# Performance work log

Measured on AMD Instinct MI355X. Metric: run time of the kernel, lower is better.

Reference implementation:

```python
import jax, jax.numpy as jnp
import numpy as np

DIM = 512
HEADS = 8
DIM_HEAD = 64
HIDDEN = HEADS * DIM_HEAD
SCALE = DIM_HEAD ** -0.5


def rmsnorm_ch(x, g):
    # F.normalize over channel dim (axis=1), then * g * sqrt(C)
    # x: [b, c, l], g: [c]
    n = jnp.maximum(jnp.linalg.norm(x, axis=1, keepdims=True), 1e-12)
    c = x.shape[1]
    return (x / n) * g[None, :, None] * (c ** 0.5)


def setup_inputs() -> dict:
    key = jax.random.key(0)
    ks = jax.random.split(key, 6)
    b, l = 8, 4096
    x = jax.random.normal(ks[0], (b, DIM, l), dtype=jnp.float32)
    g_in = jnp.ones((DIM,), dtype=jnp.float32)
    # conv1d kernel_size=1 == matmul; kaiming-ish init scale
    w_qkv = jax.random.normal(ks[1], (3 * HIDDEN, DIM), dtype=jnp.float32) * (1.0 / np.sqrt(DIM))
    w_out = jax.random.normal(ks[2], (DIM, HIDDEN), dtype=jnp.float32) * (1.0 / np.sqrt(HIDDEN))
    b_out = jax.random.normal(ks[3], (DIM,), dtype=jnp.float32) * 0.01
    g_out = jnp.ones((DIM,), dtype=jnp.float32)
    return {"x": x, "g_in": g_in, "w_qkv": w_qkv, "w_out": w_out, "b_out": b_out, "g_out": g_out}


def reference(x, g_in, w_qkv, w_out, b_out, g_out):
    b, c, l = x.shape
    residual = x
    xn = rmsnorm_ch(x, g_in)                       # [b, c, l]
    qkv = jnp.einsum('oc,bcl->bol', w_qkv, xn)     # [b, 3*hidden, l]
    q, k, v = jnp.split(qkv, 3, axis=1)            # each [b, hidden, l]
    def to_heads(t):
        return t.reshape(b, HEADS, DIM_HEAD, l)    # [b, h, d, l]
    q, k, v = to_heads(q), to_heads(k), to_heads(v)
    q = jax.nn.softmax(q, axis=2) * SCALE          # softmax over head-dim d
    k = jax.nn.softmax(k, axis=3)                  # softmax over sequence l
    context = jnp.einsum('bhdn,bhen->bhde', k, v)  # [b, h, d, e]
    out = jnp.einsum('bhde,bhdn->bhen', context, q)  # [b, h, e, l]
    out = out.reshape(b, HIDDEN, l)
    o = jnp.einsum('ch,bhl->bcl', w_out, out) + b_out[None, :, None]
    o = rmsnorm_ch(o, g_out)
    return o + residual
```

## Files before the change

kernel.cpp:

```cpp
#include <hip/hip_runtime.h>


#define BB 8
#define CC 512
#define LL 4096
#define HH 8
#define DH 64
#define TC 1536

__device__ __constant__ const float SQRT_C = 22.62741699796952f;
#define SCALE_Q 0.125f

typedef unsigned short bfr_t;
typedef __attribute__((ext_vector_type(8))) short short8;
typedef __attribute__((ext_vector_type(4))) float f32x4;
typedef __attribute__((ext_vector_type(16))) float f32x16;

__device__ __forceinline__ float bf2f(bfr_t v) {
  union { unsigned u; float f; } c; c.u = ((unsigned)v) << 16; return c.f;
}
__device__ __forceinline__ bfr_t f2bf(float f) {
  union { float f; unsigned u; } c; c.f = f;
  unsigned u = c.u + 0x7fffu + ((c.u >> 16) & 1u);
  return (bfr_t)(u >> 16);
}

__device__ __forceinline__ void load_lds16(const bfr_t* g, short* l) {
  __builtin_amdgcn_global_load_lds(
      (const __attribute__((address_space(1))) void*)g,
      (__attribute__((address_space(3))) void*)l, 16, 0, 0);
}

__global__ __launch_bounds__(256) void conv_bf16_2(
    const float* __restrict__ in1, bfr_t* __restrict__ o1, int n1,
    const float* __restrict__ in2, bfr_t* __restrict__ o2, int n2) {
  int i8 = (blockIdx.x * 256 + threadIdx.x) * 8;
  const float* src;
  bfr_t* dst;
  if (i8 < n1) { src = in1 + i8; dst = o1 + i8; }
  else {
    int j8 = i8 - n1;
    if (j8 >= n2) return;
    src = in2 + j8; dst = o2 + j8;
  }
  f32x4 a = *(const f32x4*)src;
  f32x4 b = *(const f32x4*)(src + 4);
  union { short s[8]; f32x4 v; } pk;
#pragma unroll
  for (int u = 0; u < 4; ++u) { pk.s[u] = (short)f2bf(a[u]); pk.s[u + 4] = (short)f2bf(b[u]); }
  *(f32x4*)dst = pk.v;
}

__global__ __launch_bounds__(256) void fused_norm_transpose(
    const float* __restrict__ x, const float* __restrict__ g,
    bfr_t* __restrict__ xt) {
  __shared__ float tile[64][65];
  __shared__ float red[4][64];
  __shared__ float invn_s[64];
  int b = blockIdx.y, l0 = blockIdx.x * 64;
  int t = threadIdx.x, ll = t & 63, cg = t >> 6;
  const float* xb = x + (size_t)b * CC * LL + l0;
  float vals[8][16];
  float ss = 0.f;
#pragma unroll
  for (int ch = 0; ch < 8; ++ch) {
    int c0 = ch * 64;
#pragma unroll
    for (int i = 0; i < 16; ++i) {
      int c = i * 4 + cg;
      float v = xb[(size_t)(c0 + c) * LL + ll];
      vals[ch][i] = v;
      ss += v * v;
    }
  }
  red[cg][ll] = ss;
  __syncthreads();
  if (cg == 0) {
    float s = red[0][ll] + red[1][ll] + red[2][ll] + red[3][ll];
    invn_s[ll] = SQRT_C / fmaxf(sqrtf(s), 1e-12f);
  }
  __syncthreads();
  int lw = t >> 2, ccw = (t & 3) * 16;
  float iv = invn_s[lw];
#pragma unroll
  for (int ch = 0; ch < 8; ++ch) {
    int c0 = ch * 64;
#pragma unroll
    for (int i = 0; i < 16; ++i) tile[i * 4 + cg][ll] = vals[ch][i];
    __syncthreads();
    union { short s[16]; f32x4 v[2]; } pk;
#pragma unroll
    for (int u = 0; u < 16; ++u) {
      int c = ccw + u;
      pk.s[u] = (short)f2bf(tile[c][lw] * g[c0 + c] * iv);
    }
    bfr_t* dst = xt + ((size_t)b * LL + l0 + lw) * CC + c0 + ccw;
    *(f32x4*)dst = pk.v[0];
    *(f32x4*)(dst + 8) = pk.v[1];
    __syncthreads();
  }
}

#define NT 8

__device__ __forceinline__ void stage_half(const bfr_t* g, short* l, int wid) {
  load_lds16(g + (size_t)wid * 8192,        l + wid * 1024);
  load_lds16(g + (size_t)wid * 8192 + 4096, l + wid * 1024 + 512);
}

#define CFENCE asm volatile("" ::: "memory")
#define PHASE_MID()                                          \
  do { CFENCE; __builtin_amdgcn_s_barrier();                 \
       asm volatile("s_waitcnt lgkmcnt(0)" ::: "memory");    \
       __builtin_amdgcn_sched_barrier(0); } while (0)
#define PHASE_END()                                          \
  do { CFENCE; __builtin_amdgcn_s_barrier(); CFENCE; } while (0)

#define DSR(dst, addr, lit) \
  asm volatile("ds_read_b128 %0, %1 offset:" lit : "=v"(dst) : "v"(addr))

#define LOAD_A0() do {                       \
    DSR(a_reg[0], aAs0, "0");                \
    DSR(a_reg[1], aAs1, "0");                \
    DSR(a_reg[2], aAs0, "2048");             \
    DSR(a_reg[3], aAs1, "2048");             \
    DSR(a_reg[4], aAs0, "4096");             \
    DSR(a_reg[5], aAs1, "4096");             \
    DSR(a_reg[6], aAs0, "6144");             \
    DSR(a_reg[7], aAs1, "6144"); } while (0)

#define LOAD_A1() do {                       \
    DSR(a_reg[0], aAs0, "8192");             \
    DSR(a_reg[1], aAs1, "8192");             \
    DSR(a_reg[2], aAs0, "10240");            \
    DSR(a_reg[3], aAs1, "10240");            \
    DSR(a_reg[4], aAs0, "12288");            \
    DSR(a_reg[5], aAs1, "12288");            \
    DSR(a_reg[6], aAs0, "14336");            \
    DSR(a_reg[7], aAs1, "14336"); } while (0)

#define LOAD_B0() do {                       \
    DSR(b_reg[0][0], bBs0, "0");             \
    DSR(b_reg[0][1], bBs1, "0");             \
    DSR(b_reg[0][2], bBs0, "2048");          \
    DSR(b_reg[0][3], bBs1, "2048"); } while (0)

#define LOAD_B1() do {                       \
    DSR(b_reg[1][0], bBs0, "4096");          \
    DSR(b_reg[1][1], bBs1, "4096");          \
    DSR(b_reg[1][2], bBs0, "6144");          \
    DSR(b_reg[1][3], bBs1, "6144"); } while (0)

#define MMA_Q(QM, QN) do {                                                   \
    _Pragma("unroll") for (int i_ = 0; i_ < 4; ++i_) {                       \
      _Pragma("unroll") for (int j_ = 0; j_ < 2; ++j_) {                     \
        acc[(QM) * 4 + i_][(QN) * 2 + j_] =                                  \
            __builtin_amdgcn_mfma_f32_16x16x32_bf16(                         \
                a_reg[i_ * 2 + 0], b_reg[QN][j_ * 2 + 0],                    \
                acc[(QM) * 4 + i_][(QN) * 2 + j_], 0, 0, 0);                 \
        acc[(QM) * 4 + i_][(QN) * 2 + j_] =                                  \
            __builtin_amdgcn_mfma_f32_16x16x32_bf16(                         \
                a_reg[i_ * 2 + 1], b_reg[QN][j_ * 2 + 1],                    \
                acc[(QM) * 4 + i_][(QN) * 2 + j_], 0, 0, 0);                 \
      } } } while (0)

__global__ __launch_bounds__(512, 2) void gemm256(
    const bfr_t* __restrict__ A, const bfr_t* __restrict__ Bt,
    bfr_t* __restrict__ Cout, const float* __restrict__ bias, int M) {
  __shared__ short lds[65536];
  short* As = lds;
  short* Bs = lds + 32768;

  int nwg = gridDim.x;
  int gy = M >> 8;
  int bid = blockIdx.x;
  int logical = (bid & 7) * (nwg >> 3) + (bid >> 3);
  int perz = (LL / 256) * gy;
  int bz = logical / perz;
  int rem = logical - bz * perz;
  int bx = rem / gy;
  int by = rem - bx * gy;

  int m0 = by * 256, n0 = bx * 256;
  int t = threadIdx.x, lane = t & 63, wid = t >> 6;
  int quad = lane >> 4, r16 = lane & 15;
  int wm = wid >> 2, wn = wid & 3;
  int soff = (lane >> 3) * 512 + (((lane & 7) ^ (lane >> 3)) * 8);
  int slot0 = (quad ^ (lane & 7)) * 8;
  int slot1 = ((4 + quad) ^ (lane & 7)) * 8;

  unsigned lb = (unsigned)(uintptr_t)(__attribute__((address_space(3))) short*)lds;
  unsigned aA0_0 = lb + (unsigned)(wm * 16384 + r16 * 128 + slot0 * 2);
  unsigned aA0_1 = lb + (unsigned)(wm * 16384 + r16 * 128 + slot1 * 2);
  unsigned aA1_0 = aA0_0 + 32768u;
  unsigned aA1_1 = aA0_1 + 32768u;
  unsigned bbase = 65536u + (unsigned)((wn >> 1) * 16384 + ((wn & 1) * 64 + r16) * 128);
  unsigned bB0_0 = lb + bbase + (unsigned)(slot0 * 2);
  unsigned bB0_1 = lb + bbase + (unsigned)(slot1 * 2);
  unsigned bB1_0 = bB0_0 + 32768u;
  unsigned bB1_1 = bB0_1 + 32768u;

  const bfr_t* pA0 = A + (size_t)m0 * 512 + soff;
  const bfr_t* pA1 = pA0 + (size_t)128 * 512;
  const bfr_t* pB0 = Bt + (size_t)bz * LL * 512 + (size_t)n0 * 512 + soff;
  const bfr_t* pB1 = pB0 + (size_t)128 * 512;

  f32x4 acc[8][4] = {};
  short8 a_reg[8];
  short8 b_reg[2][4];

  stage_half(pA0, As, wid);
  stage_half(pA1, As + 8192, wid);
  stage_half(pB0, Bs, wid);
  stage_half(pB1, Bs + 8192, wid);
  stage_half(pA0 + 64, As + 16384, wid);
  stage_half(pA1 + 64, As + 24576, wid);
  stage_half(pB0 + 64, Bs + 16384, wid);
  stage_half(pB1 + 64, Bs + 24576, wid);
  asm volatile("s_waitcnt vmcnt(8)" ::: "memory");
  CFENCE; __builtin_amdgcn_s_barrier(); CFENCE;

#pragma unroll
  for (int kt = 0; kt < NT; ++kt) {
    const int buf = kt & 1;
    const unsigned aAs0 = buf ? aA1_0 : aA0_0;
    const unsigned aAs1 = buf ? aA1_1 : aA0_1;
    const unsigned bBs0 = buf ? bB1_0 : bB0_0;
    const unsigned bBs1 = buf ? bB1_1 : bB0_1;
    LOAD_A0();
    LOAD_B0();
    LOAD_B1();
    if (kt >= 1 && kt <= NT - 2)
      stage_half(pA1 + (kt + 1) * 64, As + (((kt + 1) & 1) * 2 + 1) * 8192, wid);
    PHASE_MID();
    __builtin_amdgcn_s_setprio(1);
    MMA_Q(0, 0);
    MMA_Q(0, 1);
    __builtin_amdgcn_s_setprio(0);
    PHASE_END();
    LOAD_A1();
    if (kt <= NT - 3) {
      stage_half(pB0 + (kt + 2) * 64, Bs + (buf * 2) * 8192, wid);
      stage_half(pB1 + (kt + 2) * 64, Bs + (buf * 2 + 1) * 8192, wid);
      stage_half(pA0 + (kt + 2) * 64, As + (buf * 2) * 8192, wid);
    }
    PHASE_MID();
    __builtin_amdgcn_s_setprio(1);
    MMA_Q(1, 1);
    MMA_Q(1, 0);
    __builtin_amdgcn_s_setprio(0);
    __builtin_amdgcn_sched_barrier(0);
    if (kt <= NT - 3)      { asm volatile("s_waitcnt vmcnt(6)" ::: "memory"); }
    else if (kt == NT - 2) { asm volatile("s_waitcnt vmcnt(0)" ::: "memory"); }
    CFENCE; __builtin_amdgcn_s_barrier(); CFENCE;
  }

  bfr_t* Cb = Cout + (size_t)bz * M * LL;
  int crow = m0 + wm * 128 + quad * 4;
  int ccol = n0 + wn * 64 + r16;
#pragma unroll
  for (int am = 0; am < 8; ++am) {
    int rbase = crow + (am >> 2) * 64 + (am & 3) * 16;
#pragma unroll
    for (int reg = 0; reg < 4; ++reg) {
      int row = rbase + reg;
      float bi = bias ? bias[row] : 0.f;
#pragma unroll
      for (int an = 0; an < 4; ++an) {
        int col = ccol + (an >> 1) * 32 + (an & 1) * 16;
        Cb[(size_t)row * LL + col] = f2bf(acc[am][an][reg] + bi);
      }
    }
  }
}

__global__ __launch_bounds__(256) void context_mfma(
    const bfr_t* __restrict__ qkv, float* __restrict__ ctx_p,
    float* __restrict__ ksum_p) {
  __shared__ float red[4][4096];
  int s = blockIdx.x, bh = blockIdx.y;
  int b = bh >> 3, h = bh & 7;
  int t = threadIdx.x, lane = t & 63, wid = t >> 6;
  int quad = lane >> 4, r = lane & 15;
  const bfr_t* kb = qkv + ((size_t)b * TC + 512 + h * 64) * LL;
  const bfr_t* vb = qkv + ((size_t)b * TC + 1024 + h * 64) * LL;
  int n_base = s * 512 + wid * 128;
  f32x4 acc[4][4] = {};
  float ps[4] = {};
#pragma unroll
  for (int ks = 0; ks < 4; ++ks) {
    int n0 = n_base + ks * 32;
    short8 af[4], bf8[4];
#pragma unroll
    for (int i = 0; i < 4; ++i) {
      union { short s[8]; short8 v8; } uk;
      uk.v8 = *(const short8*)&kb[(size_t)(i * 16 + r) * LL + n0 + quad * 8];
#pragma unroll
      for (int jj = 0; jj < 8; ++jj) {
        float e = __expf(bf2f((bfr_t)uk.s[jj]));
        uk.s[jj] = (short)f2bf(e);
        ps[i] += e;
      }
      af[i] = uk.v8;
      bf8[i] = *(const short8*)&vb[(size_t)(i * 16 + r) * LL + n0 + quad * 8];
    }
#pragma unroll
    for (int i = 0; i < 4; ++i)
#pragma unroll
      for (int j = 0; j < 4; ++j)
        acc[i][j] = __builtin_amdgcn_mfma_f32_16x16x32_bf16(af[i], bf8[j],
                                                            acc[i][j], 0, 0, 0);
  }
#pragma unroll
  for (int i = 0; i < 4; ++i) {
    ps[i] += __shfl_xor(ps[i], 16, 64);
    ps[i] += __shfl_xor(ps[i], 32, 64);
  }
  if (quad == 0) {
#pragma unroll
    for (int i = 0; i < 4; ++i) red[wid][i * 16 + r] = ps[i];
  }
  __syncthreads();
  if (t < 64)
    ksum_p[((size_t)bh * 8 + s) * 64 + t] =
        red[0][t] + red[1][t] + red[2][t] + red[3][t];
  __syncthreads();
#pragma unroll
  for (int i = 0; i < 4; ++i)
#pragma unroll
    for (int j = 0; j < 4; ++j)
#pragma unroll
      for (int reg = 0; reg < 4; ++reg)
        red[wid][(i * 16 + quad * 4 + reg) * 64 + j * 16 + r] = acc[i][j][reg];
  __syncthreads();
  float* out = ctx_p + ((size_t)bh * 8 + s) * 4096;
#pragma unroll
  for (int u = 0; u < 16; ++u) {
    int idx = u * 256 + t;
    out[idx] = red[0][idx] + red[1][idx] + red[2][idx] + red[3][idx];
  }
}

__global__ __launch_bounds__(256) void context_reduce(
    const float* __restrict__ ctx_p, const float* __restrict__ ksum_p,
    bfr_t* __restrict__ ctx_bf) {
  __shared__ float zinv[64];
  int bh = blockIdx.x;
  int t = threadIdx.x;
  if (t < 64) {
    float s = 0.f;
#pragma unroll
    for (int s8 = 0; s8 < 8; ++s8) s += ksum_p[((size_t)bh * 8 + s8) * 64 + t];
    zinv[t] = 1.f / s;
  }
  __syncthreads();
#pragma unroll
  for (int i = 0; i < 16; ++i) {
    int idx = i * 256 + t;
    int d = idx >> 6;
    float sum = 0.f;
#pragma unroll
    for (int s = 0; s < 8; ++s) sum += ctx_p[((size_t)bh * 8 + s) * 4096 + idx];
    ctx_bf[(size_t)bh * 4096 + idx] = f2bf(sum * zinv[d]);
  }
}

__global__ __launch_bounds__(256) void apply_fused(
    const bfr_t* __restrict__ qkv, const bfr_t* __restrict__ ctx_bf,
    bfr_t* __restrict__ out_t) {
  int b = blockIdx.z, h = blockIdx.y;
  int t = threadIdx.x, lane = t & 63, wid = t >> 6;
  int quad = lane >> 4, r = lane & 15;
  int n0 = blockIdx.x * 256 + wid * 64;
  const bfr_t* qb = qkv + ((size_t)b * TC + h * 64) * LL;
  const bfr_t* cb = ctx_bf + (size_t)(b * HH + h) * 4096;
  float v[4][16];
  float pm[4];
#pragma unroll
  for (int i = 0; i < 4; ++i) {
    pm[i] = -1e30f;
#pragma unroll
    for (int ks = 0; ks < 2; ++ks)
#pragma unroll
      for (int jj = 0; jj < 8; ++jj) {
        float q = bf2f(qb[(size_t)(ks * 32 + quad * 8 + jj) * LL + n0 + i * 16 + r]);
        v[i][ks * 8 + jj] = q;
        pm[i] = fmaxf(pm[i], q);
      }
  }
#pragma unroll
  for (int i = 0; i < 4; ++i) {
    pm[i] = fmaxf(pm[i], __shfl_xor(pm[i], 16, 64));
    pm[i] = fmaxf(pm[i], __shfl_xor(pm[i], 32, 64));
  }
  float psum[4];
#pragma unroll
  for (int i = 0; i < 4; ++i) {
    float s = 0.f;
#pragma unroll
    for (int u = 0; u < 16; ++u) { v[i][u] = __expf(v[i][u] - pm[i]); s += v[i][u]; }
    psum[i] = s;
  }
#pragma unroll
  for (int i = 0; i < 4; ++i) {
    psum[i] += __shfl_xor(psum[i], 16, 64);
    psum[i] += __shfl_xor(psum[i], 32, 64);
  }
  short8 af[2][4];
#pragma unroll
  for (int i = 0; i < 4; ++i) {
    float sc = SCALE_Q / psum[i];
#pragma unroll
    for (int ks = 0; ks < 2; ++ks) {
      union { short s[8]; short8 v8; } u;
#pragma unroll
      for (int jj = 0; jj < 8; ++jj) u.s[jj] = (short)f2bf(v[i][ks * 8 + jj] * sc);
      af[ks][i] = u.v8;
    }
  }
  short8 bfrag[2][4];
#pragma unroll
  for (int ks = 0; ks < 2; ++ks)
#pragma unroll
    for (int j = 0; j < 4; ++j) {
      union { short s[8]; short8 v8; } u;
#pragma unroll
      for (int jj = 0; jj < 8; ++jj)
        u.s[jj] = (short)cb[(ks * 32 + quad * 8 + jj) * 64 + j * 16 + r];
      bfrag[ks][j] = u.v8;
    }
  f32x4 acc[4][4] = {};
#pragma unroll
  for (int ks = 0; ks < 2; ++ks)
#pragma unroll
    for (int i = 0; i < 4; ++i)
#pragma unroll
      for (int j = 0; j < 4; ++j)
        acc[i][j] = __builtin_amdgcn_mfma_f32_16x16x32_bf16(af[ks][i], bfrag[ks][j],
                                                            acc[i][j], 0, 0, 0);
  bfr_t* dst = out_t + (size_t)b * LL * 512 + h * 64;
#pragma unroll
  for (int i = 0; i < 4; ++i)
#pragma unroll
    for (int reg = 0; reg < 4; ++reg) {
      int row = n0 + i * 16 + quad * 4 + reg;
#pragma unroll
      for (int j = 0; j < 4; ++j)
        dst[(size_t)row * 512 + j * 16 + r] = f2bf(acc[i][j][reg]);
    }
}

__global__ __launch_bounds__(256) void final_norm_res(
    const bfr_t* __restrict__ o, const float* __restrict__ g,
    const float* __restrict__ x, float* __restrict__ out) {
  __shared__ float red[4][64];
  __shared__ float invn[64];
  int b = blockIdx.y, l0 = blockIdx.x * 64;
  int t = threadIdx.x, ll = t & 63, cg = t >> 6;
  const bfr_t* ob = o + (size_t)b * CC * LL + l0 + ll;
  unsigned pk[64];
  float ss = 0.f;
#pragma unroll
  for (int i = 0; i < 64; ++i) {
    int c = cg * 128 + 2 * i;
    unsigned u0 = ob[(size_t)c * LL];
    unsigned u1 = ob[(size_t)(c + 1) * LL];
    float v0 = bf2f((bfr_t)u0), v1 = bf2f((bfr_t)u1);
    ss += v0 * v0 + v1 * v1;
    pk[i] = u0 | (u1 << 16);
  }
  red[cg][ll] = ss;
  __syncthreads();
  if (cg == 0) {
    float s = red[0][ll] + red[1][ll] + red[2][ll] + red[3][ll];
    invn[ll] = SQRT_C / fmaxf(sqrtf(s), 1e-12f);
  }
  __syncthreads();
  float iv = invn[ll];
  const float* xb = x + (size_t)b * CC * LL + l0 + ll;
  float* outb = out + (size_t)b * CC * LL + l0 + ll;
#pragma unroll
  for (int i = 0; i < 64; ++i) {
    int c = cg * 128 + 2 * i;
    float v0 = bf2f((bfr_t)(pk[i] & 0xffffu));
    float v1 = bf2f((bfr_t)(pk[i] >> 16));
    outb[(size_t)c * LL] = v0 * g[c] * iv + xb[(size_t)c * LL];
    outb[(size_t)(c + 1) * LL] = v1 * g[c + 1] * iv + xb[(size_t)(c + 1) * LL];
  }
}

extern "C" void kernel_launch(void* const* d_in, const int* in_sizes, int n_in,
                              void* d_out, int out_size, void* d_ws,
                              size_t ws_size, hipStream_t stream) {
  const float* x     = (const float*)d_in[0];
  const float* g_in  = (const float*)d_in[1];
  const float* w_qkv = (const float*)d_in[2];
  const float* w_out = (const float*)d_in[3];
  const float* b_out = (const float*)d_in[4];
  const float* g_out = (const float*)d_in[5];
  float* out = (float*)d_out;

  char* ws = (char*)d_ws;
  const size_t off_wqkv  = 0;
  const size_t off_wout  = 1572864;
  const size_t off_ksump = 2097152;
  const size_t off_ctx   = 2260992;
  const size_t off_ctxp  = 3309568;
  const size_t off_xt    = 11698176;
  const size_t off_qkv   = 45252608;
  const size_t ws_need   = 145915904;
  if (ws_size < ws_need) return;

  bfr_t* wqkv_bf = (bfr_t*)(ws + off_wqkv);
  bfr_t* wout_bf = (bfr_t*)(ws + off_wout);
  float* ksum_p  = (float*)(ws + off_ksump);
  bfr_t* ctx_bf  = (bfr_t*)(ws + off_ctx);
  float* ctxp    = (float*)(ws + off_ctxp);
  bfr_t* xt      = (bfr_t*)(ws + off_xt);
  bfr_t* qkv     = (bfr_t*)(ws + off_qkv);
  bfr_t* o_bf    = (bfr_t*)(ws + off_qkv);

  conv_bf16_2<<<dim3((1536 * 512 + 512 * 512) / 8 / 256), 256, 0, stream>>>(
      w_qkv, wqkv_bf, 1536 * 512, w_out, wout_bf, 512 * 512);
  fused_norm_transpose<<<dim3(LL / 64, BB), 256, 0, stream>>>(x, g_in, xt);
  gemm256<<<dim3((LL / 256) * (TC / 256) * BB), 512, 0, stream>>>(wqkv_bf, xt, qkv, nullptr, TC);
  context_mfma<<<dim3(8, BB * HH), 256, 0, stream>>>(qkv, ctxp, ksum_p);
  context_reduce<<<dim3(BB * HH), 256, 0, stream>>>(ctxp, ksum_p, ctx_bf);
  apply_fused<<<dim3(LL / 256, HH, BB), 256, 0, stream>>>(qkv, ctx_bf, xt);
  gemm256<<<dim3((LL / 256) * (CC / 256) * BB), 512, 0, stream>>>(wout_bf, xt, o_bf, b_out, CC);
  final_norm_res<<<dim3(LL / 64, BB), 256, 0, stream>>>(o_bf, g_out, x, out);
}
```

Measured before the change: 284.9 us.

## Software-pipeline LDS fragment reads under MFMA with double-buffered registers in gemm256

Restructures the gemm256 main loop into fully unrolled even/odd tile macros that keep two register sets for A and B fragments. Each LDS read for the next sub-block is issued right before the MFMA group that uses the current registers, so LDS latency hides behind matrix math. The per-tile pair of barriers becomes one barrier, and all global-to-LDS staging for a tile is issued together after it. The cost is higher VGPR pressure from the extra fragment registers and a full vmcnt(0) wait per tile, which can shorten how far global loads run ahead.

```diff
diff --git a/kernel.cpp b/kernel.cpp
--- a/kernel.cpp
+++ b/kernel.cpp
@@ -14,7 +14,6 @@
 typedef unsigned short bfr_t;
 typedef __attribute__((ext_vector_type(8))) short short8;
 typedef __attribute__((ext_vector_type(4))) float f32x4;
-typedef __attribute__((ext_vector_type(16))) float f32x16;
 
 __device__ __forceinline__ float bf2f(bfr_t v) {
   union { unsigned u; float f; } c; c.u = ((unsigned)v) << 16; return c.f;
@@ -109,60 +108,75 @@
 }
 
 #define CFENCE asm volatile("" ::: "memory")
-#define PHASE_MID()                                          \
-  do { CFENCE; __builtin_amdgcn_s_barrier();                 \
-       asm volatile("s_waitcnt lgkmcnt(0)" ::: "memory");    \
-       __builtin_amdgcn_sched_barrier(0); } while (0)
-#define PHASE_END()                                          \
-  do { CFENCE; __builtin_amdgcn_s_barrier(); CFENCE; } while (0)
-
-#define DSR(dst, addr, lit) \
-  asm volatile("ds_read_b128 %0, %1 offset:" lit : "=v"(dst) : "v"(addr))
-
-#define LOAD_A0() do {                       \
-    DSR(a_reg[0], aAs0, "0");                \
-    DSR(a_reg[1], aAs1, "0");                \
-    DSR(a_reg[2], aAs0, "2048");             \
-    DSR(a_reg[3], aAs1, "2048");             \
-    DSR(a_reg[4], aAs0, "4096");             \
-    DSR(a_reg[5], aAs1, "4096");             \
-    DSR(a_reg[6], aAs0, "6144");             \
-    DSR(a_reg[7], aAs1, "6144"); } while (0)
-
-#define LOAD_A1() do {                       \
-    DSR(a_reg[0], aAs0, "8192");             \
-    DSR(a_reg[1], aAs1, "8192");             \
-    DSR(a_reg[2], aAs0, "10240");            \
-    DSR(a_reg[3], aAs1, "10240");            \
-    DSR(a_reg[4], aAs0, "12288");            \
-    DSR(a_reg[5], aAs1, "12288");            \
-    DSR(a_reg[6], aAs0, "14336");            \
-    DSR(a_reg[7], aAs1, "14336"); } while (0)
-
-#define LOAD_B0() do {                       \
-    DSR(b_reg[0][0], bBs0, "0");             \
-    DSR(b_reg[0][1], bBs1, "0");             \
-    DSR(b_reg[0][2], bBs0, "2048");          \
-    DSR(b_reg[0][3], bBs1, "2048"); } while (0)
-
-#define LOAD_B1() do {                       \
-    DSR(b_reg[1][0], bBs0, "4096");          \
-    DSR(b_reg[1][1], bBs1, "4096");          \
-    DSR(b_reg[1][2], bBs0, "6144");          \
-    DSR(b_reg[1][3], bBs1, "6144"); } while (0)
-
-#define MMA_Q(QM, QN) do {                                                   \
-    _Pragma("unroll") for (int i_ = 0; i_ < 4; ++i_) {                       \
+#define LGKM0 asm volatile("s_waitcnt lgkmcnt(0)" ::: "memory")
+#define VMC0  asm volatile("s_waitcnt vmcnt(0)" ::: "memory")
+#define SB    __builtin_amdgcn_sched_barrier(0)
+#define BAR   do { CFENCE; __builtin_amdgcn_s_barrier(); CFENCE; } while (0)
+#define PRIO1 __builtin_amdgcn_s_setprio(1)
+#define PRIO0 __builtin_amdgcn_s_setprio(0)
+
+#define DSR(dst, addr, LIT) \
+  asm volatile("ds_read_b128 %0, %1 offset:" #LIT : "=v"(dst) : "v"(addr))
+
+#define RD_A(S, L0, L1, L2, L3) do {           \
+    DSR(S[0], aAs0, L0); DSR(S[1], aAs1, L0);  \
+    DSR(S[2], aAs0, L1); DSR(S[3], aAs1, L1);  \
+    DSR(S[4], aAs0, L2); DSR(S[5], aAs1, L2);  \
+    DSR(S[6], aAs0, L3); DSR(S[7], aAs1, L3); } while (0)
+#define RD_B(S, L0, L1) do {                   \
+    DSR(S[0], bBs0, L0); DSR(S[1], bBs1, L0);  \
+    DSR(S[2], bBs0, L1); DSR(S[3], bBs1, L1); } while (0)
+
+#define MMA8(QM, QN, AS, BS) do {                                            \
+    _Pragma("unroll") for (int i_ = 0; i_ < 4; ++i_)                         \
       _Pragma("unroll") for (int j_ = 0; j_ < 2; ++j_) {                     \
-        acc[(QM) * 4 + i_][(QN) * 2 + j_] =                                  \
-            __builtin_amdgcn_mfma_f32_16x16x32_bf16(                         \
-                a_reg[i_ * 2 + 0], b_reg[QN][j_ * 2 + 0],                    \
-                acc[(QM) * 4 + i_][(QN) * 2 + j_], 0, 0, 0);                 \
-        acc[(QM) * 4 + i_][(QN) * 2 + j_] =                                  \
-            __builtin_amdgcn_mfma_f32_16x16x32_bf16(                         \
-                a_reg[i_ * 2 + 1], b_reg[QN][j_ * 2 + 1],                    \
-                acc[(QM) * 4 + i_][(QN) * 2 + j_], 0, 0, 0);                 \
-      } } } while (0)
+        acc[(QM)*4+i_][(QN)*2+j_] = __builtin_amdgcn_mfma_f32_16x16x32_bf16( \
+            AS[i_*2+0], BS[j_*2+0], acc[(QM)*4+i_][(QN)*2+j_], 0, 0, 0);     \
+        acc[(QM)*4+i_][(QN)*2+j_] = __builtin_amdgcn_mfma_f32_16x16x32_bf16( \
+            AS[i_*2+1], BS[j_*2+1], acc[(QM)*4+i_][(QN)*2+j_], 0, 0, 0);     \
+      }                                                                      \
+  } while (0)
+
+#define STAGE_T(J, D) do {                                                   \
+    stage_half(pA0 + (J) * 64, As + (D) * 16384, wid);                       \
+    stage_half(pA1 + (J) * 64, As + (D) * 16384 + 8192, wid);                \
+    stage_half(pB0 + (J) * 64, Bs + (D) * 16384, wid);                       \
+    stage_half(pB1 + (J) * 64, Bs + (D) * 16384 + 8192, wid);                \
+  } while (0)
+
+#define TILE_E(KT) do {                                                      \
+                                      \
+    PRIO1; RD_B(bS1, 4096, 6144); MMA8(0, 0, aS0, bS0); PRIO0; LGKM0; SB;    \
+                                      \
+    PRIO1; RD_A(aS1, 8192, 10240, 12288, 14336); MMA8(0, 1, aS0, bS1);       \
+    PRIO0; LGKM0; SB;                                                        \
+         \
+    if ((KT) < 7) { VMC0; }                                                  \
+    BAR;                                                                     \
+    if ((KT) <= 5) STAGE_T((KT) + 2, 0);                                     \
+    PRIO1;                                                                   \
+    if ((KT) < 7) RD_A(aS0, 32768, 34816, 36864, 38912);                     \
+    MMA8(1, 1, aS1, bS1); PRIO0; LGKM0; SB;                                  \
+            \
+    PRIO1; MMA8(1, 0, aS1, bS0); PRIO0;                                      \
+    if ((KT) < 7) RD_B(bS0, 32768, 34816);                                   \
+    LGKM0; SB;                                                               \
+  } while (0)
+
+#define TILE_O(KT) do {                                                      \
+    PRIO1; RD_B(bS1, 36864, 38912); MMA8(0, 0, aS0, bS0); PRIO0; LGKM0; SB;  \
+    PRIO1; RD_A(aS1, 40960, 43008, 45056, 47104); MMA8(0, 1, aS0, bS1);      \
+    PRIO0; LGKM0; SB;                                                        \
+    if ((KT) < 7) { VMC0; }                                                  \
+    BAR;                                                                     \
+    if ((KT) <= 5) STAGE_T((KT) + 2, 1);                                     \
+    PRIO1;                                                                   \
+    if ((KT) < 7) RD_A(aS0, 0, 2048, 4096, 6144);                            \
+    MMA8(1, 1, aS1, bS1); PRIO0; LGKM0; SB;                                  \
+    PRIO1; MMA8(1, 0, aS1, bS0); PRIO0;                                      \
+    if ((KT) < 7) RD_B(bS0, 0, 2048);                                        \
+    LGKM0; SB;                                                               \
+  } while (0)
 
 __global__ __launch_bounds__(512, 2) void gemm256(
     const bfr_t* __restrict__ A, const bfr_t* __restrict__ Bt,
@@ -190,15 +204,11 @@
   int slot1 = ((4 + quad) ^ (lane & 7)) * 8;
 
   unsigned lb = (unsigned)(uintptr_t)(__attribute__((address_space(3))) short*)lds;
-  unsigned aA0_0 = lb + (unsigned)(wm * 16384 + r16 * 128 + slot0 * 2);
-  unsigned aA0_1 = lb + (unsigned)(wm * 16384 + r16 * 128 + slot1 * 2);
-  unsigned aA1_0 = aA0_0 + 32768u;
-  unsigned aA1_1 = aA0_1 + 32768u;
+  unsigned aAs0 = lb + (unsigned)(wm * 16384 + r16 * 128 + slot0 * 2);
+  unsigned aAs1 = lb + (unsigned)(wm * 16384 + r16 * 128 + slot1 * 2);
   unsigned bbase = 65536u + (unsigned)((wn >> 1) * 16384 + ((wn & 1) * 64 + r16) * 128);
-  unsigned bB0_0 = lb + bbase + (unsigned)(slot0 * 2);
-  unsigned bB0_1 = lb + bbase + (unsigned)(slot1 * 2);
-  unsigned bB1_0 = bB0_0 + 32768u;
-  unsigned bB1_1 = bB0_1 + 32768u;
+  unsigned bBs0 = lb + bbase + (unsigned)(slot0 * 2);
+  unsigned bBs1 = lb + bbase + (unsigned)(slot1 * 2);
 
   const bfr_t* pA0 = A + (size_t)m0 * 512 + soff;
   const bfr_t* pA1 = pA0 + (size_t)128 * 512;
@@ -206,54 +216,19 @@
   const bfr_t* pB1 = pB0 + (size_t)128 * 512;
 
   f32x4 acc[8][4] = {};
-  short8 a_reg[8];
-  short8 b_reg[2][4];
-
-  stage_half(pA0, As, wid);
-  stage_half(pA1, As + 8192, wid);
-  stage_half(pB0, Bs, wid);
-  stage_half(pB1, Bs + 8192, wid);
-  stage_half(pA0 + 64, As + 16384, wid);
-  stage_half(pA1 + 64, As + 24576, wid);
-  stage_half(pB0 + 64, Bs + 16384, wid);
-  stage_half(pB1 + 64, Bs + 24576, wid);
+  short8 aS0[8], aS1[8];
+  short8 bS0[4], bS1[4];
+
+  STAGE_T(0, 0);
+  STAGE_T(1, 1);
   asm volatile("s_waitcnt vmcnt(8)" ::: "memory");
-  CFENCE; __builtin_amdgcn_s_barrier(); CFENCE;
-
-#pragma unroll
-  for (int kt = 0; kt < NT; ++kt) {
-    const int buf = kt & 1;
-    const unsigned aAs0 = buf ? aA1_0 : aA0_0;
-    const unsigned aAs1 = buf ? aA1_1 : aA0_1;
-    const unsigned bBs0 = buf ? bB1_0 : bB0_0;
-    const unsigned bBs1 = buf ? bB1_1 : bB0_1;
-    LOAD_A0();
-    LOAD_B0();
-    LOAD_B1();
-    if (kt >= 1 && kt <= NT - 2)
-      stage_half(pA1 + (kt + 1) * 64, As + (((kt + 1) & 1) * 2 + 1) * 8192, wid);
-    PHASE_MID();
-    __builtin_amdgcn_s_setprio(1);
-    MMA_Q(0, 0);
-    MMA_Q(0, 1);
-    __builtin_amdgcn_s_setprio(0);
-    PHASE_END();
-    LOAD_A1();
-    if (kt <= NT - 3) {
-      stage_half(pB0 + (kt + 2) * 64, Bs + (buf * 2) * 8192, wid);
-      stage_half(pB1 + (kt + 2) * 64, Bs + (buf * 2 + 1) * 8192, wid);
-      stage_half(pA0 + (kt + 2) * 64, As + (buf * 2) * 8192, wid);
-    }
-    PHASE_MID();
-    __builtin_amdgcn_s_setprio(1);
-    MMA_Q(1, 1);
-    MMA_Q(1, 0);
-    __builtin_amdgcn_s_setprio(0);
-    __builtin_amdgcn_sched_barrier(0);
-    if (kt <= NT - 3)      { asm volatile("s_waitcnt vmcnt(6)" ::: "memory"); }
-    else if (kt == NT - 2) { asm volatile("s_waitcnt vmcnt(0)" ::: "memory"); }
-    CFENCE; __builtin_amdgcn_s_barrier(); CFENCE;
-  }
+  BAR;
+  RD_A(aS0, 0, 2048, 4096, 6144);
+  RD_B(bS0, 0, 2048);
+  LGKM0; SB;
+
+  TILE_E(0); TILE_O(1); TILE_E(2); TILE_O(3);
+  TILE_E(4); TILE_O(5); TILE_E(6); TILE_O(7);
 
   bfr_t* Cb = Cout + (size_t)bz * M * LL;
   int crow = m0 + wm * 128 + quad * 4;
```

Measured after the change: 280.9 us. Within noise of the previous version (-1.4%).
